# Kernel optimization log

Measured on AMD Instinct MI355X. Metric: run time of the kernel, lower is better.

## Reference

```python
import jax, jax.numpy as jnp
import numpy as np

N, T, E, B = 50000, 16, 800000, 2000
EMB, ENC, DEC, OUT_LEN = 32, 64, 128, 25
NEG_SLOPE = 0.1
BN_EPS = 1e-5


def lrelu(x):
    return jnp.where(x >= 0, x, NEG_SLOPE * x)


def gru_encode(xs, Wih, Whh, bih, bhh):
    # xs: [T, N, in] -> final hidden [N, H]   (torch GRU gate order: r, z, n)
    H = Whh.shape[1]

    def step(h, x_t):
        gi = x_t @ Wih.T + bih
        gh = h @ Whh.T + bhh
        i_r, i_z, i_n = jnp.split(gi, 3, axis=-1)
        h_r, h_z, h_n = jnp.split(gh, 3, axis=-1)
        r = jax.nn.sigmoid(i_r + h_r)
        z = jax.nn.sigmoid(i_z + h_z)
        n = jnp.tanh(i_n + r * h_n)
        return (1.0 - z) * n + z * h, None

    h0 = jnp.zeros((xs.shape[1], H), xs.dtype)
    hT, _ = jax.lax.scan(step, h0, xs)
    return hT


def lstm_layer(xs, Wih, Whh, bih, bhh):
    # xs: [T, B, in] -> outputs [T, B, H]   (torch LSTM gate order: i, f, g, o)
    H = Whh.shape[1]

    def step(carry, x_t):
        h, c = carry
        g = x_t @ Wih.T + bih + h @ Whh.T + bhh
        i, f, gg, o = jnp.split(g, 4, axis=-1)
        c = jax.nn.sigmoid(f) * c + jax.nn.sigmoid(i) * jnp.tanh(gg)
        h = jax.nn.sigmoid(o) * jnp.tanh(c)
        return (h, c), h

    z0 = jnp.zeros((xs.shape[1], H), xs.dtype)
    _, hs = jax.lax.scan(step, (z0, z0), xs)
    return hs


def cgconv(x, src, dst, edge_attr, Wf, bf, Ws, bs, gamma, beta, mean, var):
    # PyG CGConv: z = [x_i, x_j, e]; msg = sigmoid(lin_f(z)) * softplus(lin_s(z));
    # out = x + BN(scatter_add(msg, i))
    z = jnp.concatenate([x[dst], x[src], edge_attr], axis=-1)  # [E, 2*ENC+2]
    msg = jax.nn.sigmoid(z @ Wf.T + bf) * jax.nn.softplus(z @ Ws.T + bs)
    agg = jax.ops.segment_sum(msg, dst, num_segments=N)  # [N, ENC]
    agg = (agg - mean) * jax.lax.rsqrt(var + BN_EPS) * gamma + beta
    return x + agg


def setup_inputs() -> dict:
    key = jax.random.key(0)
    ks = jax.random.split(key, 32)

    def rn(k, shape, scale=0.1):
        return jax.random.normal(k, shape, jnp.float32) * scale

    inp = {}
    inp["x"] = jax.random.normal(ks[0], (N, T, 2), jnp.float32)
    inp["edge_index"] = jax.random.randint(ks[1], (2, E), 0, N)
    inp["edge_attr"] = jax.random.normal(ks[2], (E, 2), jnp.float32)
    inp["target_index"] = jnp.sort(jax.random.randint(ks[3], (B,), 0, N))
    inp["W_ip"] = rn(ks[4], (EMB, 2)); inp["b_ip"] = jnp.zeros((EMB,), jnp.float32)
    inp["gru_Wih"] = rn(ks[5], (3 * ENC, EMB)); inp["gru_Whh"] = rn(ks[6], (3 * ENC, ENC))
    inp["gru_bih"] = jnp.zeros((3 * ENC,), jnp.float32); inp["gru_bhh"] = jnp.zeros((3 * ENC,), jnp.float32)
    inp["W_dyn"] = rn(ks[7], (ENC, ENC)); inp["b_dyn"] = jnp.zeros((ENC,), jnp.float32)
    Z = 2 * ENC + 2
    for i, base in ((1, 8), (2, 14)):
        inp[f"cg{i}_Wf"] = rn(ks[base], (ENC, Z)); inp[f"cg{i}_bf"] = jnp.zeros((ENC,), jnp.float32)
        inp[f"cg{i}_Ws"] = rn(ks[base + 1], (ENC, Z)); inp[f"cg{i}_bs"] = jnp.zeros((ENC,), jnp.float32)
        inp[f"cg{i}_gamma"] = jnp.ones((ENC,), jnp.float32); inp[f"cg{i}_beta"] = jnp.zeros((ENC,), jnp.float32)
        inp[f"cg{i}_mean"] = jnp.zeros((ENC,), jnp.float32); inp[f"cg{i}_var"] = jnp.ones((ENC,), jnp.float32)
    inp["W_nbrs"] = rn(ks[20], (ENC, ENC)); inp["b_nbrs"] = jnp.zeros((ENC,), jnp.float32)
    inp["lstm0_Wih"] = rn(ks[21], (4 * DEC, 2 * ENC)); inp["lstm0_Whh"] = rn(ks[22], (4 * DEC, DEC))
    inp["lstm0_bih"] = jnp.zeros((4 * DEC,), jnp.float32); inp["lstm0_bhh"] = jnp.zeros((4 * DEC,), jnp.float32)
    inp["lstm1_Wih"] = rn(ks[23], (4 * DEC, DEC)); inp["lstm1_Whh"] = rn(ks[24], (4 * DEC, DEC))
    inp["lstm1_bih"] = jnp.zeros((4 * DEC,), jnp.float32); inp["lstm1_bhh"] = jnp.zeros((4 * DEC,), jnp.float32)
    inp["W_op"] = rn(ks[25], (2, DEC)); inp["b_op"] = jnp.zeros((2,), jnp.float32)
    return inp


def reference(x, edge_index, edge_attr, target_index, W_ip, b_ip,
              gru_Wih, gru_Whh, gru_bih, gru_bhh, W_dyn, b_dyn,
              cg1_Wf, cg1_bf, cg1_Ws, cg1_bs, cg1_gamma, cg1_beta, cg1_mean, cg1_var,
              cg2_Wf, cg2_bf, cg2_Ws, cg2_bs, cg2_gamma, cg2_beta, cg2_mean, cg2_var,
              W_nbrs, b_nbrs,
              lstm0_Wih, lstm0_Whh, lstm0_bih, lstm0_bhh,
              lstm1_Wih, lstm1_Whh, lstm1_bih, lstm1_bhh, W_op, b_op):
    src, dst = edge_index[0], edge_index[1]
    # --- history encoder (GRU) ---
    h = lrelu(x @ W_ip.T + b_ip)                                  # [N, T, EMB]
    hT = gru_encode(h.transpose(1, 0, 2), gru_Wih, gru_Whh, gru_bih, gru_bhh)  # [N, ENC]
    hist = lrelu(lrelu(hT) @ W_dyn.T + b_dyn)                     # [N, ENC]
    # --- CGConv interaction x2 ---
    f = cgconv(hist, src, dst, edge_attr, cg1_Wf, cg1_bf, cg1_Ws, cg1_bs,
               cg1_gamma, cg1_beta, cg1_mean, cg1_var)
    f = cgconv(f, src, dst, edge_attr, cg2_Wf, cg2_bf, cg2_Ws, cg2_bs,
               cg2_gamma, cg2_beta, cg2_mean, cg2_var)
    tar = lrelu(f[target_index] @ W_nbrs.T + b_nbrs)              # [B, ENC]
    enc = jnp.concatenate([hist[target_index], tar], axis=-1)     # [B, 2*ENC]
    # --- LSTM decoder over repeated encoding ---
    xs = jnp.broadcast_to(enc, (OUT_LEN,) + enc.shape)            # [OUT_LEN, B, 2*ENC]
    hs = lstm_layer(xs, lstm0_Wih, lstm0_Whh, lstm0_bih, lstm0_bhh)
    hs = lstm_layer(hs, lstm1_Wih, lstm1_Whh, lstm1_bih, lstm1_bhh)
    fut = hs.transpose(1, 0, 2) @ W_op.T + b_op                   # [B, OUT_LEN, 2]
    return fut
```

## Files before the change

### kernel.cpp

```cpp
#include <hip/hip_runtime.h>
#include <hip/hip_fp16.h>
#include <math.h>

#define NN   50000
#define TT   16
#define EE   800000
#define BB   2000
#define EMBD 32
#define ENC  64
#define DEC  128
#define OUTL 25
#define BN_EPS 1e-5f

typedef short v8s __attribute__((ext_vector_type(8)));
typedef float v4f __attribute__((ext_vector_type(4)));
#define MFMA16(a,b,c) __builtin_amdgcn_mfma_f32_16x16x32_bf16((a),(b),(c),0,0,0)

__device__ __forceinline__ float lrelu(float v){ return v >= 0.f ? v : 0.1f*v; }
__device__ __forceinline__ float fsig(float v){ return __builtin_amdgcn_rcpf(1.f + __expf(-v)); }
__device__ __forceinline__ float ftanh(float v){ return 2.f*__builtin_amdgcn_rcpf(1.f + __expf(-2.f*v)) - 1.f; }
__device__ __forceinline__ float fsoftplus(float v){
    return v > 15.f ? v : __logf(1.f + __expf(v));
}

__device__ __forceinline__ unsigned short f2bf(float f){
    unsigned u = __float_as_uint(f);
    u = u + 0x7FFFu + ((u>>16)&1u);
    return (unsigned short)(u>>16);
}
__device__ __forceinline__ float bf2f(unsigned short s){ return __uint_as_float(((unsigned)s)<<16); }

__device__ __forceinline__ void tsplit(float v, unsigned short& hi, unsigned short& lo){
    unsigned u = __float_as_uint(v);
    hi = (unsigned short)(u >> 16);
    float r = v - __uint_as_float(u & 0xFFFF0000u);
    lo = (unsigned short)(__float_as_uint(r) >> 16);
}

__device__ __forceinline__ v8s as_v8s(int4 v){
    union { int4 i; v8s s; } u; u.i = v; return u.s;
}

__device__ __forceinline__ void cvt8(const float* p, v8s& hi, v8s& lo){
    float4 a0 = *(const float4*)p;
    float4 a1 = *(const float4*)(p+4);
    float av[8] = {a0.x,a0.y,a0.z,a0.w,a1.x,a1.y,a1.z,a1.w};
#pragma unroll
    for (int j=0;j<8;j++){
        unsigned short h = f2bf(av[j]);
        hi[j] = (short)h;
        lo[j] = (short)f2bf(av[j] - bf2f(h));
    }
}
__device__ __forceinline__ void lrelu_resplit(v8s hh, v8s hl, v8s& oh, v8s& ol){
#pragma unroll
    for (int j=0;j<8;j++){
        float v = bf2f((unsigned short)hh[j]) + bf2f((unsigned short)hl[j]);
        float a = lrelu(v);
        unsigned short h = f2bf(a);
        oh[j] = (short)h;
        ol[j] = (short)f2bf(a - bf2f(h));
    }
}

__device__ __forceinline__ void pf_item(const float* W, int K, int KB, int i,
                                        unsigned short* out){
    int l = i & 63, fb = i >> 6;
    int kb = fb % KB, nt = fb / KB;
    int n = nt*16 + (l&15);
    int k0 = kb*32 + ((l>>4)*8);
#pragma unroll
    for (int j=0;j<8;j++) out[i*8+j] = f2bf(W[(size_t)n*K + k0 + j]);
}
__device__ __forceinline__ void phl_item(const float* W, int K, int KB, int i,
                                         unsigned short* hi, unsigned short* lo){
    int l = i & 63, fb = i >> 6;
    int kb = fb % KB, nt = fb / KB;
    int n = nt*16 + (l&15);
    int k0 = kb*32 + ((l>>4)*8);
#pragma unroll
    for (int j=0;j<8;j++){
        float v = W[(size_t)n*K + k0 + j];
        unsigned short h = f2bf(v);
        hi[i*8+j] = h;
        lo[i*8+j] = f2bf(v - bf2f(h));
    }
}
__device__ __forceinline__ void pcat_item(const float* Wa, const float* Wb,
                                          int K1, int K, int KB, int i,
                                          unsigned short* out){
    int l = i & 63, fb = i >> 6;
    int kb = fb % KB, nt = fb / KB;
    int n = nt*16 + (l&15);
    int k0 = kb*32 + ((l>>4)*8);
#pragma unroll
    for (int j=0;j<8;j++){
        int k = k0 + j;
        float v = (k < K1) ? Wa[(size_t)n*K1 + k] : Wb[(size_t)n*(K-K1) + (k-K1)];
        out[i*8+j] = f2bf(v);
    }
}
__device__ __forceinline__ void pproj_item(const float* Wf, const float* Ws, int i,
                                           unsigned short* hi, unsigned short* lo){
    int l = i & 63, fb = i >> 6;
    int kb = fb & 1, nt = fb >> 1;
    int n = nt*16 + (l&15);
    int d = n >> 6, c = n & 63;
    const float* W = (d < 2) ? Wf : Ws;
    int k0 = (d&1)*64 + kb*32 + ((l>>4)*8);
#pragma unroll
    for (int j=0;j<8;j++){
        float v = W[c*130 + k0 + j];
        unsigned short h = f2bf(v);
        hi[i*8+j] = h;
        lo[i*8+j] = f2bf(v - bf2f(h));
    }
}

__global__ void pack_all(
    const float* __restrict__ gWih, const float* __restrict__ gWhh,
    const float* __restrict__ Wdyn,
    const float* __restrict__ l0Whh, const float* __restrict__ l1Wih,
    const float* __restrict__ l1Whh, const float* __restrict__ l0Wih,
    const float* __restrict__ c1Wf, const float* __restrict__ c1Ws,
    const float* __restrict__ c2Wf, const float* __restrict__ c2Ws,
    unsigned short* __restrict__ pWih, unsigned short* __restrict__ pWhh,
    unsigned short* __restrict__ pWdyn,
    unsigned short* __restrict__ B0h, unsigned short* __restrict__ B1h,
    unsigned short* __restrict__ P1h, unsigned short* __restrict__ P1l,
    unsigned short* __restrict__ P2h, unsigned short* __restrict__ P2l,
    unsigned short* __restrict__ GIh, unsigned short* __restrict__ GIl,
    int* __restrict__ cnt, int* __restrict__ gtot)
{
    int i = blockIdx.x*256 + threadIdx.x;
    if (i < 768){ pf_item(gWih, 32, 1, i, pWih); return; }   i -= 768;
    if (i < 1536){ pf_item(gWhh, 64, 2, i, pWhh); return; }  i -= 1536;
    if (i < 512){ pf_item(Wdyn, 64, 2, i, pWdyn); return; }  i -= 512;
    if (i < 8192){ pcat_item(l0Whh, l0Whh, 128, 128, 4, i, B0h); return; } i -= 8192;
    if (i < 16384){ pcat_item(l1Wih, l1Whh, 128, 256, 8, i, B1h); return; } i -= 16384;
    if (i < 2048){ pproj_item(c1Wf, c1Ws, i, P1h, P1l); return; } i -= 2048;
    if (i < 2048){ pproj_item(c2Wf, c2Ws, i, P2h, P2l); return; } i -= 2048;
    if (i < 8192){ phl_item(l0Wih, 128, 4, i, GIh, GIl); return; } i -= 8192;
    if (i < NN){ cnt[i] = 0; return; } i -= NN;
    if (i < 1){ gtot[0] = 0; return; }
}
#define PACK_TOTAL (768+1536+512+8192+16384+2048+2048+8192+NN+1)

__global__ __launch_bounds__(256) void encoder_mfma(
    const float* __restrict__ x,
    const float* __restrict__ Wip, const float* __restrict__ bip,
    const unsigned short* __restrict__ pWih,
    const unsigned short* __restrict__ pWhh,
    const float* __restrict__ bih, const float* __restrict__ bhh,
    const unsigned short* __restrict__ pWdyn,
    const float* __restrict__ bdyn,
    float* __restrict__ hist)
{
    __shared__ unsigned short efh[4*512], efl[4*512];
    __shared__ unsigned short hfh[2][1024], hfl[2][1024];
    const int tid = threadIdx.x;
    const int l   = tid & 63;
    const int w   = tid >> 6;
    const int ln  = l & 15, q = l >> 4;
    const int blk = blockIdx.x;
    const int rsw = ((l>>1)&7)<<3;

    for (int i = tid; i < 1024; i += 256){
        hfh[0][i]=0; hfl[0][i]=0; hfh[1][i]=0; hfl[1][i]=0;
    }

    const int k0 = tid & 31;
    const int mb = tid >> 5;
    const float ew0 = Wip[2*k0], ew1 = Wip[2*k0+1], ebk = bip[k0];
    const int ebase = (k0>>3)*128 + (k0&7);
    const float2* xr0 = (const float2*)(x + (size_t)(blk*16 + 2*mb    )*32);
    const float2* xr1 = (const float2*)(x + (size_t)(blk*16 + 2*mb + 1)*32);

    const int c = w*16 + ln;
    const float bR  = bih[c]       + bhh[c];
    const float bZ  = bih[64 + c]  + bhh[64 + c];
    const float bNI = bih[128 + c];
    const float bNH = bhh[128 + c];
    float hprev[4] = {0.f,0.f,0.f,0.f};

    const v8s* FIH = (const v8s*)pWih;
    const v8s* FHH = (const v8s*)pWhh;
    const v8s* FDY = (const v8s*)pWdyn;
    const int wbase = (c>>5)*512 + (16*((c&31)>>3))*8 + (c&7);
    __syncthreads();

    int p = 0;
#pragma unroll 1
    for (int tb = 0; tb < 4; tb++){
#pragma unroll
        for (int ts = 0; ts < 4; ts++){
            int t = tb*4 + ts;
            float2 xv0 = xr0[t], xv1 = xr1[t];
            float e0 = lrelu(ew0*xv0.x + ew1*xv0.y + ebk);
            float e1 = lrelu(ew0*xv1.x + ew1*xv1.y + ebk);
            unsigned short h_, l_;
            tsplit(e0, h_, l_);
            efh[ts*512 + ebase + (2*mb  )*8] = h_;
            efl[ts*512 + ebase + (2*mb  )*8] = l_;
            tsplit(e1, h_, l_);
            efh[ts*512 + ebase + (2*mb+1)*8] = h_;
            efl[ts*512 + ebase + (2*mb+1)*8] = l_;
        }
        __syncthreads();
#pragma unroll 1
        for (int ts = 0; ts < 4; ts++){
            v8s eh  = *(const v8s*)&efh[ts*512 + l*8];
            v8s el  = *(const v8s*)&efl[ts*512 + l*8];
            v8s h0h = *(const v8s*)&hfh[p][(l*8) ^ rsw];
            v8s h0l = *(const v8s*)&hfl[p][(l*8) ^ rsw];
            v8s h1h = *(const v8s*)&hfh[p][512 + ((l*8) ^ rsw)];
            v8s h1l = *(const v8s*)&hfl[p][512 + ((l*8) ^ rsw)];

            v4f aR = {bR,bR,bR,bR};
            v4f aZ = {bZ,bZ,bZ,bZ};
            v4f aNI= {bNI,bNI,bNI,bNI};
            v4f aNH= {bNH,bNH,bNH,bNH};
            v8s b;
            b = FIH[(w   )*64 + l];    aR = MFMA16(eh,b,aR);  aR = MFMA16(el,b,aR);
            b = FHH[(w*2+0)*64+l];     aR = MFMA16(h0h,b,aR); aR = MFMA16(h0l,b,aR);
            b = FHH[(w*2+1)*64+l];     aR = MFMA16(h1h,b,aR); aR = MFMA16(h1l,b,aR);
            b = FIH[(4+w )*64 + l];    aZ = MFMA16(eh,b,aZ);  aZ = MFMA16(el,b,aZ);
            b = FHH[((4+w)*2+0)*64+l]; aZ = MFMA16(h0h,b,aZ); aZ = MFMA16(h0l,b,aZ);
            b = FHH[((4+w)*2+1)*64+l]; aZ = MFMA16(h1h,b,aZ); aZ = MFMA16(h1l,b,aZ);
            b = FIH[(8+w )*64 + l];    aNI= MFMA16(eh,b,aNI); aNI= MFMA16(el,b,aNI);
            b = FHH[((8+w)*2+0)*64+l]; aNH= MFMA16(h0h,b,aNH);aNH= MFMA16(h0l,b,aNH);
            b = FHH[((8+w)*2+1)*64+l]; aNH= MFMA16(h1h,b,aNH);aNH= MFMA16(h1l,b,aNH);

#pragma unroll
            for (int i = 0; i < 4; i++){
                float r_ = fsig(aR[i]);
                float z_ = fsig(aZ[i]);
                float nn_ = ftanh(aNI[i] + r_*aNH[i]);
                float hn = nn_ + z_*(hprev[i] - nn_);
                hprev[i] = hn;
                int row = q*4 + i;
                int off = (wbase + row*8) ^ ((((row)>>1)&7)<<3);
                unsigned short hh_, hl_;
                tsplit(hn, hh_, hl_);
                hfh[1-p][off] = hh_;
                hfl[1-p][off] = hl_;
            }
            __syncthreads();
            p ^= 1;
        }
    }
    {
        v8s a0h,a0l,a1h,a1l;
        lrelu_resplit(*(const v8s*)&hfh[p][(l*8) ^ rsw],
                      *(const v8s*)&hfl[p][(l*8) ^ rsw],       a0h, a0l);
        lrelu_resplit(*(const v8s*)&hfh[p][512 + ((l*8) ^ rsw)],
                      *(const v8s*)&hfl[p][512 + ((l*8) ^ rsw)], a1h, a1l);
        const int nt = w;
        float bb = bdyn[nt*16 + ln];
        v4f acc = {bb,bb,bb,bb};
        v8s b;
        b = FDY[(nt*2+0)*64 + l]; acc = MFMA16(a0h,b,acc); acc = MFMA16(a0l,b,acc);
        b = FDY[(nt*2+1)*64 + l]; acc = MFMA16(a1h,b,acc); acc = MFMA16(a1l,b,acc);
#pragma unroll
        for (int i = 0; i < 4; i++){
            hist[(size_t)(blk*16 + q*4 + i)*64 + nt*16 + ln] = lrelu(acc[i]);
        }
    }
}

#define PROJ_ACC(NT, ACC) { \
    v8s bh0_ = FH[((NT)*2+0)*64 + l], bl0_ = FL[((NT)*2+0)*64 + l]; \
    v8s bh1_ = FH[((NT)*2+1)*64 + l], bl1_ = FL[((NT)*2+1)*64 + l]; \
    ACC = MFMA16(ah0,bh0_,ACC); ACC = MFMA16(al0,bh0_,ACC); ACC = MFMA16(ah0,bl0_,ACC); \
    ACC = MFMA16(ah1,bh1_,ACC); ACC = MFMA16(al1,bh1_,ACC); ACC = MFMA16(ah1,bl1_,ACC); }

__global__ __launch_bounds__(256) void proj_mfma(
    const float* __restrict__ xin,
    const unsigned short* __restrict__ Bh, const unsigned short* __restrict__ Bl,
    float* __restrict__ Af, float* __restrict__ As,
    unsigned* __restrict__ BP)
{
    __shared__ float sx[64*68];
    const int tid = threadIdx.x;
    const int l = tid & 63;
    const int w = tid >> 6;
    const int ln = l & 15, q = l >> 4;
    const int n0 = blockIdx.x*64;

    for (int i=tid;i<64*16;i+=256){
        int nn = i>>4, f4 = i&15;
        float4 v = {0.f,0.f,0.f,0.f};
        if (n0+nn < NN) v = ((const float4*)(xin + (size_t)(n0+nn)*64))[f4];
        *(float4*)&sx[nn*68 + f4*4] = v;
    }
    __syncthreads();

    v8s ah0,al0,ah1,al1;
    cvt8(&sx[(w*16+ln)*68 +      q*8], ah0, al0);
    cvt8(&sx[(w*16+ln)*68 + 32 + q*8], ah1, al1);

    const v8s* FH = (const v8s*)Bh;
    const v8s* FL = (const v8s*)Bl;
#pragma unroll 1
    for (int c3=0; c3<4; c3++){
        v4f aA = {0.f,0.f,0.f,0.f};
        v4f aS = aA, aF = aA, aB = aA;
        PROJ_ACC(c3,      aA);
        PROJ_ACC(8 + c3,  aS);
        PROJ_ACC(4 + c3,  aF);
        PROJ_ACC(12 + c3, aB);
        int col = c3*16 + ln;
#pragma unroll
        for (int i=0;i<4;i++){
            int node = n0 + w*16 + q*4 + i;
            if (node < NN){
                Af[(size_t)node*64 + col] = aA[i];
                As[(size_t)node*64 + col] = aS[i];
                unsigned pf = __half_as_ushort(__float2half(aF[i]));
                unsigned ps = __half_as_ushort(__float2half(aB[i]));
                BP[(size_t)node*64 + col] = pf | (ps << 16);
            }
        }
    }
}

__global__ void count_kernel(const int* __restrict__ ei, int* __restrict__ cnt){
    int e = blockIdx.x*256 + threadIdx.x;
    if (e < EE) atomicAdd(&cnt[ei[EE+e]], 1);
}

__global__ void alloc_kernel(const int* __restrict__ cnt, int* __restrict__ gtot,
                             int* __restrict__ off, int* __restrict__ cur){
    int n = blockIdx.x*256 + threadIdx.x;
    if (n >= NN) return;
    int c = cnt[n];
    int s = atomicAdd(gtot, c);
    off[n] = s;
    cur[n] = s;
}

__global__ void scatter_kernel(const int* __restrict__ ei, const float* __restrict__ ea,
                               int* __restrict__ cur, int4* __restrict__ recS){
    int e = blockIdx.x*256 + threadIdx.x;
    if (e >= EE) return;
    int d = ei[EE+e];
    int p = atomicAdd(&cur[d], 1);
    int4 r;
    r.x = ei[e];
    r.y = __float_as_int(ea[2*(size_t)e]);
    r.z = __float_as_int(ea[2*(size_t)e+1]);
    r.w = 0;
    recS[p] = r;
}

__global__ __launch_bounds__(256) void cg_agg(
    const float* __restrict__ xin,
    const int4* __restrict__ recS,
    const int* __restrict__ off, const int* __restrict__ cnt,
    const float* __restrict__ Wf, const float* __restrict__ bf,
    const float* __restrict__ Ws, const float* __restrict__ bs,
    const float* __restrict__ Af, const float* __restrict__ As,
    const unsigned* __restrict__ BP,
    const float* __restrict__ gamma, const float* __restrict__ beta,
    const float* __restrict__ mean, const float* __restrict__ var,
    float* __restrict__ outp)
{
    const int tid = threadIdx.x;
    const int c = tid & 63, wid = tid >> 6;
    const int n = blockIdx.x*4 + wid;
    if (n >= NN) return;

    const float wf0 = Wf[c*130+128], wf1 = Wf[c*130+129], bfc = bf[c];
    const float ws0 = Ws[c*130+128], ws1 = Ws[c*130+129], bsc = bs[c];
    const float afd = Af[(size_t)n*64+c] + bfc, asd = As[(size_t)n*64+c] + bsc;
    const unsigned* BPc = BP + c;

    float acc = 0.f;
    int i = off[n];
    const int i1 = i + cnt[n];
#pragma unroll 1
    for (; i+1 < i1; i += 2){
        int4 r0 = recS[i], r1 = recS[i+1];
        float e00 = __int_as_float(r0.y), e01 = __int_as_float(r0.z);
        float e10 = __int_as_float(r1.y), e11 = __int_as_float(r1.z);
        unsigned pv0 = BPc[(size_t)r0.x*64];
        unsigned pv1 = BPc[(size_t)r1.x*64];
        float bf0v = __half2float(__ushort_as_half((unsigned short)(pv0 & 0xFFFFu)));
        float bs0v = __half2float(__ushort_as_half((unsigned short)(pv0 >> 16)));
        float bf1v = __half2float(__ushort_as_half((unsigned short)(pv1 & 0xFFFFu)));
        float bs1v = __half2float(__ushort_as_half((unsigned short)(pv1 >> 16)));
        float gf0 = afd + bf0v + wf0*e00 + wf1*e01;
        float gs0 = asd + bs0v + ws0*e00 + ws1*e01;
        float gf1 = afd + bf1v + wf0*e10 + wf1*e11;
        float gs1 = asd + bs1v + ws0*e10 + ws1*e11;
        acc += fsig(gf0)*fsoftplus(gs0);
        acc += fsig(gf1)*fsoftplus(gs1);
    }
    if (i < i1){
        int4 r0 = recS[i];
        float e00 = __int_as_float(r0.y), e01 = __int_as_float(r0.z);
        unsigned pv0 = BPc[(size_t)r0.x*64];
        float bf0v = __half2float(__ushort_as_half((unsigned short)(pv0 & 0xFFFFu)));
        float bs0v = __half2float(__ushort_as_half((unsigned short)(pv0 >> 16)));
        float gf = afd + bf0v + wf0*e00 + wf1*e01;
        float gs = asd + bs0v + ws0*e00 + ws1*e01;
        acc += fsig(gf)*fsoftplus(gs);
    }
    float bn = (acc - mean[c])*rsqrtf(var[c]+BN_EPS)*gamma[c] + beta[c];
    outp[(size_t)n*64+c] = xin[(size_t)n*64+c] + bn;
}

__global__ __launch_bounds__(256) void target_kernel(
    const float* __restrict__ hist, const float* __restrict__ f2,
    const int* __restrict__ tgt,
    const float* __restrict__ Wn, const float* __restrict__ bn_,
    float* __restrict__ enc)
{
    const int tid=threadIdx.x;
    const int c = tid&63, q = tid>>6;
    const int b = blockIdx.x*4 + q;
    if (b>=BB) return;
    const int n = tgt[b];
    float a = bn_[c];
#pragma unroll
    for (int k=0;k<ENC;k++) a += Wn[c*64+k]*f2[(size_t)n*64+k];
    enc[(size_t)b*128 + 64 + c] = lrelu(a);
    enc[(size_t)b*128 + c]      = hist[(size_t)n*64+c];
}

__global__ __launch_bounds__(512) void gi0_mfma(
    const float* __restrict__ enc,
    const unsigned short* __restrict__ GIh, const unsigned short* __restrict__ GIl,
    const float* __restrict__ bih0, const float* __restrict__ bhh0,
    float* __restrict__ gi0)
{
    __shared__ float senc[16*132];
    const int tid = threadIdx.x;
    const int l = tid & 63;
    const int w = tid >> 6;
    const int ln = l & 15, q = l >> 4;
    const int b0 = blockIdx.x*16;

    for (int i=tid;i<16*32;i+=512){
        int row = i>>5, f4 = i&31;
        *(float4*)&senc[row*132 + f4*4] = ((const float4*)(enc + (size_t)(b0+row)*128))[f4];
    }
    __syncthreads();

    v8s ah[4], al[4];
#pragma unroll
    for (int kb=0;kb<4;kb++) cvt8(&senc[ln*132 + kb*32 + q*8], ah[kb], al[kb]);

    const v8s* FH = (const v8s*)GIh;
    const v8s* FL = (const v8s*)GIl;
#pragma unroll
    for (int u=0;u<4;u++){
        int nt = w*4 + u;
        int col = nt*16 + ln;
        float bb = bih0[col] + bhh0[col];
        v4f acc = {bb,bb,bb,bb};
#pragma unroll
        for (int kb=0;kb<4;kb++){
            v8s bh = FH[(nt*4+kb)*64 + l];
            v8s bl = FL[(nt*4+kb)*64 + l];
            acc = MFMA16(ah[kb],bh,acc); acc = MFMA16(al[kb],bh,acc); acc = MFMA16(ah[kb],bl,acc);
        }
#pragma unroll
        for (int i=0;i<4;i++)
            gi0[(size_t)(b0 + q*4 + i)*512 + col] = acc[i];
    }
}

#define LMB 16
__global__ __launch_bounds__(512)
__attribute__((amdgpu_waves_per_eu(2,2)))
void lstm_mfma(
    const float* __restrict__ gi0,
    const unsigned short* __restrict__ B0h,
    const unsigned short* __restrict__ B1h,
    const float* __restrict__ bih1, const float* __restrict__ bhh1,
    float* __restrict__ h1buf)
{
    __shared__ int4 sW0[32*4*64];
    __shared__ unsigned short h0hi[2][4*512], h0lo[2][4*512];
    __shared__ unsigned short h1hi[2][4*512], h1lo[2][4*512];
    const int tid = threadIdx.x;
    const int l = tid & 63;
    const int w = tid >> 6;
    const int c = l & 15;
    const int q = l >> 4;
    const int j = w*16 + c;
    const int b0 = blockIdx.x*LMB;
    const int lsw = ((l>>1)&7)<<3;

    {
        const int4* F0 = (const int4*)B0h;
        for (int i=tid;i<32*4*64;i+=512) sW0[i] = F0[i];
    }
    for (int i=tid;i<4*512;i+=512){
        h0hi[0][i]=0; h0lo[0][i]=0; h0hi[1][i]=0; h0lo[1][i]=0;
        h1hi[0][i]=0; h1lo[0][i]=0; h1hi[1][i]=0; h1lo[1][i]=0;
    }

    int4 W1r[32];
    {
        const int4* F1 = (const int4*)B1h;
#pragma unroll
        for (int g=0;g<4;g++)
#pragma unroll
            for (int kb=0;kb<8;kb++) W1r[g*8+kb] = F1[((g*8+w)*8 + kb)*64 + l];
#pragma unroll
        for (int i=0;i<32;i++)
            asm volatile("" : "+v"(W1r[i].x), "+v"(W1r[i].y), "+v"(W1r[i].z), "+v"(W1r[i].w));
    }

    float rgi[4][4];
#pragma unroll
    for (int g=0;g<4;g++)
#pragma unroll
        for (int i=0;i<4;i++)
            rgi[g][i] = gi0[(size_t)(b0 + q*4 + i)*512 + g*128 + j];

    float b1[4];
#pragma unroll
    for (int g=0;g<4;g++) b1[g] = bih1[g*128+j] + bhh1[g*128+j];
    float c0[4] = {0,0,0,0}, c1[4] = {0,0,0,0};
    const int kbw = j>>5, qw = (j>>3)&3, jw = j&7;
    __syncthreads();

    int p = 0;
#pragma unroll 1
    for (int t=0;t<OUTL;t++){
        v4f aH[4], aL[4];
#pragma unroll
        for (int g=0;g<4;g++){
            v4f t4 = {rgi[g][0], rgi[g][1], rgi[g][2], rgi[g][3]};
            aH[g] = t4;
            v4f z = {0.f,0.f,0.f,0.f};
            aL[g] = z;
        }
#pragma unroll
        for (int kb=0;kb<4;kb++){
            v8s ah = *(const v8s*)&h0hi[p][kb*512 + ((l*8) ^ lsw)];
            v8s al = *(const v8s*)&h0lo[p][kb*512 + ((l*8) ^ lsw)];
#pragma unroll
            for (int g=0;g<4;g++){
                v8s bfr = as_v8s(sW0[((g*8+w)*4 + kb)*64 + l]);
                aH[g] = MFMA16(ah, bfr, aH[g]);
                aL[g] = MFMA16(al, bfr, aL[g]);
            }
        }
#pragma unroll
        for (int i=0;i<4;i++){
            float gi_ = aH[0][i]+aL[0][i], gf_ = aH[1][i]+aL[1][i];
            float gg_ = aH[2][i]+aL[2][i], go_ = aH[3][i]+aL[3][i];
            c0[i] = fsig(gf_)*c0[i] + fsig(gi_)*ftanh(gg_);
            float hn = fsig(go_)*ftanh(c0[i]);
            int row = q*4 + i;
            int off = (kbw*512 + (qw*16 + row)*8 + jw) ^ (((row>>1)&7)<<3);
            unsigned short h = f2bf(hn);
            h0hi[1-p][off] = h;
            h0lo[1-p][off] = f2bf(hn - bf2f(h));
        }
        __syncthreads();

        v4f bH[4], bL[4];
#pragma unroll
        for (int g=0;g<4;g++){
            v4f t4={b1[g],b1[g],b1[g],b1[g]}; bH[g]=t4;
            v4f z={0.f,0.f,0.f,0.f}; bL[g]=z;
        }
#pragma unroll
        for (int kb=0;kb<8;kb++){
            const unsigned short* hb = (kb<4) ? h0hi[1-p] : h1hi[p];
            const unsigned short* lb = (kb<4) ? h0lo[1-p] : h1lo[p];
            int kk = kb & 3;
            v8s ah = *(const v8s*)&hb[kk*512 + ((l*8) ^ lsw)];
            v8s al = *(const v8s*)&lb[kk*512 + ((l*8) ^ lsw)];
#pragma unroll
            for (int g=0;g<4;g++){
                bH[g] = MFMA16(ah, as_v8s(W1r[g*8+kb]), bH[g]);
                bL[g] = MFMA16(al, as_v8s(W1r[g*8+kb]), bL[g]);
            }
        }
        float h1new[4];
#pragma unroll
        for (int i=0;i<4;i++){
            float gi_ = bH[0][i]+bL[0][i], gf_ = bH[1][i]+bL[1][i];
            float gg_ = bH[2][i]+bL[2][i], go_ = bH[3][i]+bL[3][i];
            c1[i] = fsig(gf_)*c1[i] + fsig(gi_)*ftanh(gg_);
            h1new[i] = fsig(go_)*ftanh(c1[i]);
            int row = q*4 + i;
            int off = (kbw*512 + (qw*16 + row)*8 + jw) ^ (((row>>1)&7)<<3);
            unsigned short h = f2bf(h1new[i]);
            h1hi[1-p][off] = h;
            h1lo[1-p][off] = f2bf(h1new[i] - bf2f(h));
        }

#pragma unroll
        for (int i=0;i<4;i++){
            h1buf[((size_t)(b0 + q*4 + i)*OUTL + t)*DEC + j] = h1new[i];
        }
        p ^= 1;
    }
}

__global__ __launch_bounds__(256) void out_proj(
    const float* __restrict__ h1buf,
    const float* __restrict__ Wop, const float* __restrict__ bop,
    float* __restrict__ outp)
{
    int idx = blockIdx.x*256 + threadIdx.x;
    if (idx >= BB*OUTL) return;
    const float4* hp = (const float4*)(h1buf + (size_t)idx*DEC);
    const float4* w0 = (const float4*)Wop;
    const float4* w1 = (const float4*)(Wop + DEC);
    float a0 = 0.f, a1 = 0.f;
#pragma unroll
    for (int k=0;k<32;k++){
        float4 h = hp[k], x0 = w0[k], x1 = w1[k];
        a0 += h.x*x0.x + h.y*x0.y + h.z*x0.z + h.w*x0.w;
        a1 += h.x*x1.x + h.y*x1.y + h.z*x1.z + h.w*x1.w;
    }
    outp[(size_t)idx*2    ] = a0 + bop[0];
    outp[(size_t)idx*2 + 1] = a1 + bop[1];
}

extern "C" void kernel_launch(void* const* d_in, const int* in_sizes, int n_in,
                              void* d_out, int out_size, void* d_ws, size_t ws_size,
                              hipStream_t stream)
{
    const float* x    = (const float*)d_in[0];
    const int*   ei   = (const int*)d_in[1];
    const float* ea   = (const float*)d_in[2];
    const int*   tgt  = (const int*)d_in[3];
    const float* Wip  = (const float*)d_in[4];
    const float* bip  = (const float*)d_in[5];
    const float* gWih = (const float*)d_in[6];
    const float* gWhh = (const float*)d_in[7];
    const float* gbih = (const float*)d_in[8];
    const float* gbhh = (const float*)d_in[9];
    const float* Wdyn = (const float*)d_in[10];
    const float* bdyn = (const float*)d_in[11];
    const float* c1Wf=(const float*)d_in[12]; const float* c1bf=(const float*)d_in[13];
    const float* c1Ws=(const float*)d_in[14]; const float* c1bs=(const float*)d_in[15];
    const float* c1g =(const float*)d_in[16]; const float* c1b =(const float*)d_in[17];
    const float* c1m =(const float*)d_in[18]; const float* c1v =(const float*)d_in[19];
    const float* c2Wf=(const float*)d_in[20]; const float* c2bf=(const float*)d_in[21];
    const float* c2Ws=(const float*)d_in[22]; const float* c2bs=(const float*)d_in[23];
    const float* c2g =(const float*)d_in[24]; const float* c2b =(const float*)d_in[25];
    const float* c2m =(const float*)d_in[26]; const float* c2v =(const float*)d_in[27];
    const float* Wn  =(const float*)d_in[28]; const float* bn_ =(const float*)d_in[29];
    const float* l0Wih=(const float*)d_in[30]; const float* l0Whh=(const float*)d_in[31];
    const float* l0bih=(const float*)d_in[32]; const float* l0bhh=(const float*)d_in[33];
    const float* l1Wih=(const float*)d_in[34]; const float* l1Whh=(const float*)d_in[35];
    const float* l1bih=(const float*)d_in[36]; const float* l1bhh=(const float*)d_in[37];
    const float* Wop =(const float*)d_in[38]; const float* bop=(const float*)d_in[39];

    float* ws = (float*)d_ws;
    size_t o = 0;
    float* hist = ws + o; o += (size_t)NN*ENC;
    float* f1   = ws + o; o += (size_t)NN*ENC;
    float* f2   = ws + o; o += (size_t)NN*ENC;
    float* Af   = ws + o; o += (size_t)NN*ENC;
    float* Bfs  = ws + o; o += (size_t)NN*ENC;
    float* As   = ws + o; o += (size_t)NN*ENC;
    float* Bs   = ws + o; o += (size_t)NN*ENC;
    float* enc  = ws + o; o += (size_t)BB*2*ENC;
    float* gi0  = ws + o; o += (size_t)BB*4*DEC;
    unsigned short* pWih  = (unsigned short*)(ws + o); o += (size_t)12*64*8/2;
    unsigned short* pWhh  = (unsigned short*)(ws + o); o += (size_t)24*64*8/2;
    unsigned short* pWdyn = (unsigned short*)(ws + o); o += (size_t)8*64*8/2;
    unsigned short* B0h = (unsigned short*)(ws + o); o += (size_t)32*4*64*8/2;
    unsigned short* B1h = (unsigned short*)(ws + o); o += (size_t)32*8*64*8/2;
    unsigned short* P1h = (unsigned short*)(ws + o); o += (size_t)2048*8/2;
    unsigned short* P1l = (unsigned short*)(ws + o); o += (size_t)2048*8/2;
    unsigned short* P2h = (unsigned short*)(ws + o); o += (size_t)2048*8/2;
    unsigned short* P2l = (unsigned short*)(ws + o); o += (size_t)2048*8/2;
    unsigned short* GIh = (unsigned short*)(ws + o); o += (size_t)8192*8/2;
    unsigned short* GIl = (unsigned short*)(ws + o); o += (size_t)8192*8/2;
    int* cnt    = (int*)(ws + o); o += NN;
    int* offv   = (int*)(ws + o); o += NN+1;
    int* curv   = (int*)(ws + o); o += NN;
    int* gtot   = (int*)(ws + o); o += 1;
    o = (o + 3) & ~(size_t)3;
    int4* recS  = (int4*)(ws + o); o += (size_t)4*EE;

    unsigned* BP = (unsigned*)Bfs;

    float* h1buf = Af;

    pack_all<<<(PACK_TOTAL+255)/256, 256, 0, stream>>>(
        gWih, gWhh, Wdyn, l0Whh, l1Wih, l1Whh, l0Wih,
        c1Wf, c1Ws, c2Wf, c2Ws,
        pWih, pWhh, pWdyn, B0h, B1h, P1h, P1l, P2h, P2l, GIh, GIl, cnt, gtot);

    count_kernel<<<(EE+255)/256, 256, 0, stream>>>(ei, cnt);
    alloc_kernel<<<(NN+255)/256, 256, 0, stream>>>(cnt, gtot, offv, curv);
    scatter_kernel<<<(EE+255)/256, 256, 0, stream>>>(ei, ea, curv, recS);

    encoder_mfma<<<NN/16, 256, 0, stream>>>(x, Wip, bip, pWih, pWhh, gbih, gbhh, pWdyn, bdyn, hist);

    proj_mfma<<<(NN+63)/64, 256, 0, stream>>>(hist, P1h, P1l, Af, As, BP);
    cg_agg<<<(NN+3)/4, 256, 0, stream>>>(hist, recS, offv, cnt,
                                         c1Wf,c1bf,c1Ws,c1bs, Af, As, BP,
                                         c1g,c1b,c1m,c1v, f1);

    proj_mfma<<<(NN+63)/64, 256, 0, stream>>>(f1, P2h, P2l, Af, As, BP);
    cg_agg<<<(NN+3)/4, 256, 0, stream>>>(f1, recS, offv, cnt,
                                         c2Wf,c2bf,c2Ws,c2bs, Af, As, BP,
                                         c2g,c2b,c2m,c2v, f2);

    target_kernel<<<(BB+3)/4, 256, 0, stream>>>(hist, f2, tgt, Wn, bn_, enc);

    gi0_mfma<<<BB/16, 512, 0, stream>>>(enc, GIh, GIl, l0bih, l0bhh, gi0);

    lstm_mfma<<<BB/LMB, 512, 0, stream>>>(gi0, B0h, B1h,
                                          l1bih, l1bhh, h1buf);

    out_proj<<<(BB*OUTL+255)/256, 256, 0, stream>>>(h1buf, Wop, bop, (float*)d_out);
}
```

Baseline: 567.9 us.

## Pack CSR edge records to 8 bytes and hold LSTM layer-0 weights in registers

```diff
diff --git a/kernel.cpp b/kernel.cpp
--- a/kernel.cpp
+++ b/kernel.cpp
@@ -340,22 +340,22 @@
 }
 
 __global__ void scatter_kernel(const int* __restrict__ ei, const float* __restrict__ ea,
-                               int* __restrict__ cur, int4* __restrict__ recS){
+                               int* __restrict__ cur, int2* __restrict__ recS){
     int e = blockIdx.x*256 + threadIdx.x;
     if (e >= EE) return;
     int d = ei[EE+e];
     int p = atomicAdd(&cur[d], 1);
-    int4 r;
+    unsigned e0 = __half_as_ushort(__float2half(ea[2*(size_t)e]));
+    unsigned e1 = __half_as_ushort(__float2half(ea[2*(size_t)e+1]));
+    int2 r;
     r.x = ei[e];
-    r.y = __float_as_int(ea[2*(size_t)e]);
-    r.z = __float_as_int(ea[2*(size_t)e+1]);
-    r.w = 0;
+    r.y = (int)(e0 | (e1 << 16));
     recS[p] = r;
 }
 
 __global__ __launch_bounds__(256) void cg_agg(
     const float* __restrict__ xin,
-    const int4* __restrict__ recS,
+    const int2* __restrict__ recS,
     const int* __restrict__ off, const int* __restrict__ cnt,
     const float* __restrict__ Wf, const float* __restrict__ bf,
     const float* __restrict__ Ws, const float* __restrict__ bs,
@@ -380,9 +380,12 @@
     const int i1 = i + cnt[n];
 #pragma unroll 1
     for (; i+1 < i1; i += 2){
-        int4 r0 = recS[i], r1 = recS[i+1];
-        float e00 = __int_as_float(r0.y), e01 = __int_as_float(r0.z);
-        float e10 = __int_as_float(r1.y), e11 = __int_as_float(r1.z);
+        int2 r0 = recS[i], r1 = recS[i+1];
+        unsigned ea0 = (unsigned)r0.y, ea1 = (unsigned)r1.y;
+        float e00 = __half2float(__ushort_as_half((unsigned short)(ea0 & 0xFFFFu)));
+        float e01 = __half2float(__ushort_as_half((unsigned short)(ea0 >> 16)));
+        float e10 = __half2float(__ushort_as_half((unsigned short)(ea1 & 0xFFFFu)));
+        float e11 = __half2float(__ushort_as_half((unsigned short)(ea1 >> 16)));
         unsigned pv0 = BPc[(size_t)r0.x*64];
         unsigned pv1 = BPc[(size_t)r1.x*64];
         float bf0v = __half2float(__ushort_as_half((unsigned short)(pv0 & 0xFFFFu)));
@@ -397,8 +400,10 @@
         acc += fsig(gf1)*fsoftplus(gs1);
     }
     if (i < i1){
-        int4 r0 = recS[i];
-        float e00 = __int_as_float(r0.y), e01 = __int_as_float(r0.z);
+        int2 r0 = recS[i];
+        unsigned ea0 = (unsigned)r0.y;
+        float e00 = __half2float(__ushort_as_half((unsigned short)(ea0 & 0xFFFFu)));
+        float e01 = __half2float(__ushort_as_half((unsigned short)(ea0 >> 16)));
         unsigned pv0 = BPc[(size_t)r0.x*64];
         float bf0v = __half2float(__ushort_as_half((unsigned short)(pv0 & 0xFFFFu)));
         float bs0v = __half2float(__ushort_as_half((unsigned short)(pv0 >> 16)));
@@ -481,7 +486,6 @@
     const float* __restrict__ bih1, const float* __restrict__ bhh1,
     float* __restrict__ h1buf)
 {
-    __shared__ int4 sW0[32*4*64];
     __shared__ unsigned short h0hi[2][4*512], h0lo[2][4*512];
     __shared__ unsigned short h1hi[2][4*512], h1lo[2][4*512];
     const int tid = threadIdx.x;
@@ -493,13 +497,21 @@
     const int b0 = blockIdx.x*LMB;
     const int lsw = ((l>>1)&7)<<3;
 
-    {
-        const int4* F0 = (const int4*)B0h;
-        for (int i=tid;i<32*4*64;i+=512) sW0[i] = F0[i];
-    }
     for (int i=tid;i<4*512;i+=512){
         h0hi[0][i]=0; h0lo[0][i]=0; h0hi[1][i]=0; h0lo[1][i]=0;
         h1hi[0][i]=0; h1lo[0][i]=0; h1hi[1][i]=0; h1lo[1][i]=0;
+    }
+
+    int4 W0r[16];
+    {
+        const int4* F0 = (const int4*)B0h;
+#pragma unroll
+        for (int g=0;g<4;g++)
+#pragma unroll
+            for (int kb=0;kb<4;kb++) W0r[g*4+kb] = F0[((g*8+w)*4 + kb)*64 + l];
+#pragma unroll
+        for (int i=0;i<16;i++)
+            asm volatile("" : "+v"(W0r[i].x), "+v"(W0r[i].y), "+v"(W0r[i].z), "+v"(W0r[i].w));
     }
 
     int4 W1r[32];
@@ -545,7 +557,7 @@
             v8s al = *(const v8s*)&h0lo[p][kb*512 + ((l*8) ^ lsw)];
 #pragma unroll
             for (int g=0;g<4;g++){
-                v8s bfr = as_v8s(sW0[((g*8+w)*4 + kb)*64 + l]);
+                v8s bfr = as_v8s(W0r[g*4 + kb]);
                 aH[g] = MFMA16(ah, bfr, aH[g]);
                 aL[g] = MFMA16(al, bfr, aL[g]);
             }
@@ -665,7 +677,6 @@
     float* Af   = ws + o; o += (size_t)NN*ENC;
     float* Bfs  = ws + o; o += (size_t)NN*ENC;
     float* As   = ws + o; o += (size_t)NN*ENC;
-    float* Bs   = ws + o; o += (size_t)NN*ENC;
     float* enc  = ws + o; o += (size_t)BB*2*ENC;
     float* gi0  = ws + o; o += (size_t)BB*4*DEC;
     unsigned short* pWih  = (unsigned short*)(ws + o); o += (size_t)12*64*8/2;
@@ -684,7 +695,7 @@
     int* curv   = (int*)(ws + o); o += NN;
     int* gtot   = (int*)(ws + o); o += 1;
     o = (o + 3) & ~(size_t)3;
-    int4* recS  = (int4*)(ws + o); o += (size_t)4*EE;
+    int2* recS  = (int2*)(ws + o); o += (size_t)2*EE;
 
     unsigned* BP = (unsigned*)Bfs;
 
```

Measured after the change: 611.3 us. 7.6% more time.
